# Kernel tuning notes

Hardware: AMD Instinct MI355X
Metric: run time of the kernel (lower is better)

## Reference

```python
import jax, jax.numpy as jnp
import numpy as np
import math

# ---- static configuration (mirrors init_kwargs) ----
NQ = 8            # n_qubits (main register)
NA = 2            # n_ancilla = ceil(log2(n_select))
NSEL = 4          # n_select
DEG = 3           # degree
LAYERS = 2        # n_ansatz_layers
KLOC = 2          # k_local
LATENT = 128
B = 256
NROTS = 4 * NQ * LAYERS          # 64
GROUPS = [(s, s + 1) for s in range(NQ - KLOC + 1)]  # sliding 2-local -> 7 groups
NOBS = len(GROUPS)
KDIM = 2 ** KLOC                  # 4
C64 = jnp.complex64
TWO_PI = 2.0 * math.pi

CNOT = jnp.array([[1, 0, 0, 0], [0, 1, 0, 0], [0, 0, 0, 1], [0, 0, 1, 0]], dtype=C64)

# ---- gate matrices (theta may be traced) ----
def ry_mat(th):
    c = jnp.cos(th / 2).astype(C64); s = jnp.sin(th / 2).astype(C64)
    return jnp.stack([jnp.stack([c, -s]), jnp.stack([s, c])])

def rz_mat(th):
    return jnp.diag(jnp.stack([jnp.exp(-0.5j * th), jnp.exp(0.5j * th)])).astype(C64)

def crx_mat(th):
    c = jnp.cos(th / 2).astype(C64); isn = (-1j * jnp.sin(th / 2)).astype(C64)
    one = jnp.ones((), C64)
    m = jnp.zeros((4, 4), C64)
    m = m.at[0, 0].set(one).at[1, 1].set(one)
    m = m.at[2, 2].set(c).at[3, 3].set(c).at[2, 3].set(isn).at[3, 2].set(isn)
    return m

# ---- state-vector gate application (state: (2,)*rank, wire = axis) ----
def apply_1q(state, U, w):
    return jnp.moveaxis(jnp.tensordot(U, state, axes=((1,), (w,))), 0, w)

def apply_2q(state, U, w0, w1):
    st = jnp.tensordot(U.reshape(2, 2, 2, 2), state, axes=((2, 3), (w0, w1)))
    return jnp.moveaxis(st, (0, 1), (w0, w1))

def _sim14_ops(nq, layers):
    ops, idx = [], 0
    for _ in range(layers):
        for i in range(nq):
            ops.append(("ry", (i,), idx)); idx += 1
        for i in range(nq - 1, -1, -1):
            ops.append(("crx", (i, (i + 1) % nq), idx)); idx += 1
        for i in range(nq):
            ops.append(("ry", (i,), idx)); idx += 1
        for i in [nq - 1] + list(range(nq - 1)):
            ops.append(("crx", (i, (i - 1) % nq), idx)); idx += 1
    return ops

def apply_sim14(state, p, layers, adjoint=False):
    ops = _sim14_ops(NQ, layers)
    seq = list(reversed(ops)) if adjoint else ops
    sgn = -1.0 if adjoint else 1.0
    for kind, ws, idx in seq:
        th = sgn * p[idx]
        if kind == "ry":
            state = apply_1q(state, ry_mat(th), ws[0])
        else:
            state = apply_2q(state, crx_mat(th), ws[0], ws[1])
    return state

def pcphase(state, phi):
    # e^{+i phi} on ancilla=|0..0> subspace (first 2^NQ states in (anc, main) ordering), e^{-i phi} elsewhere
    sr = state.reshape(2 ** NQ, 2 ** NA)
    ph = jnp.where(jnp.arange(2 ** NA) == 0, jnp.exp(1j * phi), jnp.exp(-1j * phi)).astype(C64)
    return (sr * ph[None, :]).reshape(state.shape)

def prepare(state, prep_p, adjoint=False):
    if not adjoint:
        for ly in range(NA):          # n_prep_layers == n_ancilla
            for qi in range(NA):
                state = apply_1q(state, ry_mat(prep_p[ly, qi, 0]), NQ + qi)
                state = apply_1q(state, rz_mat(prep_p[ly, qi, 1]), NQ + qi)
            for i in range(NA - 1):
                state = apply_2q(state, CNOT, NQ + i, NQ + i + 1)
    else:
        for ly in reversed(range(NA)):
            for i in reversed(range(NA - 1)):
                state = apply_2q(state, CNOT, NQ + i, NQ + i + 1)
            for qi in reversed(range(NA)):
                state = apply_1q(state, rz_mat(-prep_p[ly, qi, 1]), NQ + qi)
                state = apply_1q(state, ry_mat(-prep_p[ly, qi, 0]), NQ + qi)
    return state

def select(state, ts, adjoint=False):
    # ancilla wires (NQ, NQ+1) are the trailing axes; flattened index == control value s
    sr = state.reshape((2,) * NQ + (2 ** NA,))
    for s in range(NSEL):
        sub = apply_sim14(sr[..., s], ts[s], LAYERS, adjoint=adjoint)
        sr = sr.at[..., s].set(sub)
    return sr.reshape(state.shape)

def create_hermitian(A, Bp, D, N):
    h = jnp.zeros((N, N), C64)
    count = 0
    for i in range(1, N):
        h = h.at[i - 1, i - 1].set(D[i].astype(C64))
        for j in range(i):
            h = h.at[i, j].set((A[count + j] + 1j * Bp[count + j]).astype(C64))
        count += i
    return h + h.conj().T

def simulate(ts, prep_p, sig, qff, H_all):
    # ts: (NSEL, NROTS) for one batch element
    state = jnp.zeros((2,) * (NQ + NA), C64).at[(0,) * (NQ + NA)].set(1.0)
    state = pcphase(state, sig[0])
    for k in range(DEG):
        state = prepare(state, prep_p)
        state = select(state, ts, adjoint=(k % 2 == 1))
        state = prepare(state, prep_p, adjoint=True)
        state = pcphase(state, sig[k + 1])
    state = apply_sim14(state, qff, 1)
    es = []
    for w, (a, b) in enumerate(GROUPS):
        hpsi = apply_2q(state, H_all[w], a, b)
        es.append(jnp.real(jnp.vdot(state, hpsi)))
    return jnp.stack(es).astype(jnp.float32)  # (NOBS,)

def linear(x, w, b):
    return x @ w.T + b

def sinusoidal_embedding(t, dim):
    half = dim // 2
    freqs = jnp.exp(-math.log(10000.0) * jnp.arange(half, dtype=jnp.float32) / half)
    args = t[:, None] * freqs[None]
    return jnp.concatenate([jnp.cos(args), jnp.sin(args)], axis=-1)

def _forward(z_t, t, te_w1, te_b1, te_w2, te_b2, ip_w1, ip_b1, ip_w2, ip_b2,
             prep_params, signal_angles, qff_params, A_obs, B_obs, D_obs, head_w, head_b):
    t_emb = sinusoidal_embedding(t, LATENT)
    t_emb = linear(jax.nn.silu(linear(t_emb, te_w1, te_b1)), te_w2, te_b2)
    h = jnp.concatenate([z_t, t_emb], axis=-1)
    h = linear(jax.nn.silu(linear(h, ip_w1, ip_b1)), ip_w2, ip_b2)
    ts = jax.nn.sigmoid(h).reshape(z_t.shape[0], NSEL, NROTS) * TWO_PI
    H_all = jax.vmap(lambda a, b, d: create_hermitian(a, b, d, KDIM))(A_obs, B_obs, D_obs)  # (NOBS,4,4)
    expvals = jax.vmap(simulate, in_axes=(0, None, None, None, None))(
        ts, prep_params, signal_angles, qff_params, H_all)  # (B, NOBS)
    return linear(expvals, head_w, head_b)  # (B, LATENT)

def setup_inputs() -> dict:
    key = jax.random.key(0)
    ks = jax.random.split(key, 16)
    def n(k, shape, s=0.05):
        return s * jax.random.normal(k, shape, jnp.float32)
    return {
        "z_t": jax.random.normal(ks[0], (B, LATENT), jnp.float32),
        "t": jax.random.uniform(ks[1], (B,), jnp.float32),
        "te_w1": n(ks[2], (LATENT, LATENT)), "te_b1": jnp.zeros((LATENT,), jnp.float32),
        "te_w2": n(ks[3], (LATENT, LATENT)), "te_b2": jnp.zeros((LATENT,), jnp.float32),
        "ip_w1": n(ks[4], (2 * LATENT, 2 * LATENT)), "ip_b1": jnp.zeros((2 * LATENT,), jnp.float32),
        "ip_w2": n(ks[5], (NSEL * NROTS, 2 * LATENT)), "ip_b2": jnp.zeros((NSEL * NROTS,), jnp.float32),
        "prep_params": 0.1 * jax.random.normal(ks[6], (NA, NA, 2), jnp.float32),
        "signal_angles": 0.1 * jax.random.normal(ks[7], (DEG + 1,), jnp.float32),
        "qff_params": jax.random.uniform(ks[8], (4 * NQ,), jnp.float32),
        "A_obs": 2.0 * jax.random.normal(ks[9], (NOBS, KDIM * (KDIM - 1) // 2), jnp.float32),
        "B_obs": 2.0 * jax.random.normal(ks[10], (NOBS, KDIM * (KDIM - 1) // 2), jnp.float32),
        "D_obs": 2.0 * jax.random.normal(ks[11], (NOBS, KDIM), jnp.float32),
        "head_w": n(ks[12], (LATENT, NOBS)), "head_b": jnp.zeros((LATENT,), jnp.float32),
    }

def reference(z_t, t, te_w1, te_b1, te_w2, te_b2, ip_w1, ip_b1, ip_w2, ip_b2,
              prep_params, signal_angles, qff_params, A_obs, B_obs, D_obs, head_w, head_b):
    return _forward(z_t, t, te_w1, te_b1, te_w2, te_b2, ip_w1, ip_b1, ip_w2, ip_b2,
                    prep_params, signal_angles, qff_params, A_obs, B_obs, D_obs, head_w, head_b)
```

## Files before the change

kernel.cpp:

```cpp
#include <hip/hip_runtime.h>
#include <math.h>

#define NOBS 7
#define PI_F 3.14159265358979f


typedef float v2f __attribute__((ext_vector_type(2)));

__device__ __forceinline__ v2f pk_mul(v2f a, v2f b) {
  v2f d;
  asm("v_pk_mul_f32 %0, %1, %2" : "=v"(d) : "v"(a), "v"(b));
  return d;
}
__device__ __forceinline__ v2f pk_fma(v2f a, v2f b, v2f c) {
  v2f d;
  asm("v_pk_fma_f32 %0, %1, %2, %3" : "=v"(d) : "v"(a), "v"(b), "v"(c));
  return d;
}

template<int LM>
__device__ __forceinline__ float lane_partner(float x) {
  if constexpr (LM == 1) {
    return __int_as_float(__builtin_amdgcn_mov_dpp(__float_as_int(x), 0xB1, 0xF, 0xF, true));
  } else if constexpr (LM == 2) {
    return __int_as_float(__builtin_amdgcn_mov_dpp(__float_as_int(x), 0x4E, 0xF, 0xF, true));
  } else if constexpr (LM == 4) {
    int a = __builtin_amdgcn_mov_dpp(__float_as_int(x), 0x1B, 0xF, 0xF, true);
    return __int_as_float(__builtin_amdgcn_mov_dpp(a, 0x141, 0xF, 0xF, true));
  } else if constexpr (LM == 8) {
    int a = __builtin_amdgcn_mov_dpp(__float_as_int(x), 0x141, 0xF, 0xF, true);
    return __int_as_float(__builtin_amdgcn_mov_dpp(a, 0x140, 0xF, 0xF, true));
  } else if constexpr (LM == 16) {
#if __has_builtin(__builtin_amdgcn_permlane16_swap)
    unsigned xu = __float_as_uint(x);
    auto r = __builtin_amdgcn_permlane16_swap(xu, xu, false, false);
    return (__uint_as_float(r[0]) + __uint_as_float(r[1])) - x;
#else
    return __shfl_xor(x, 16, 64);
#endif
  } else {
#if __has_builtin(__builtin_amdgcn_permlane32_swap)
    unsigned xu = __float_as_uint(x);
    auto r = __builtin_amdgcn_permlane32_swap(xu, xu, false, false);
    return (__uint_as_float(r[0]) + __uint_as_float(r[1])) - x;
#else
    return __shfl_xor(x, 32, 64);
#endif
  }
}

template<int LM>
__device__ __forceinline__ float xor_sum(float x) {
  if constexpr (LM == 16) {
#if __has_builtin(__builtin_amdgcn_permlane16_swap)
    unsigned xu = __float_as_uint(x);
    auto r = __builtin_amdgcn_permlane16_swap(xu, xu, false, false);
    return __uint_as_float(r[0]) + __uint_as_float(r[1]);
#else
    return x + __shfl_xor(x, 16, 64);
#endif
  } else if constexpr (LM == 32) {
#if __has_builtin(__builtin_amdgcn_permlane32_swap)
    unsigned xu = __float_as_uint(x);
    auto r = __builtin_amdgcn_permlane32_swap(xu, xu, false, false);
    return __uint_as_float(r[0]) + __uint_as_float(r[1]);
#else
    return x + __shfl_xor(x, 32, 64);
#endif
  } else {
    return x + lane_partner<LM>(x);
  }
}

__device__ __forceinline__ float rdlane(float v, int idx) {
  return __int_as_float(__builtin_amdgcn_readlane(__float_as_int(v), idx));
}

__device__ __forceinline__ float2 cmul(float2 a, float2 b) {
  return make_float2(a.x*b.x - a.y*b.y, a.x*b.y + a.y*b.x);
}
__device__ __forceinline__ float2 cmulc(float2 a, float2 b) {
  return make_float2(a.x*b.x + a.y*b.y, a.y*b.x - a.x*b.y);
}
__device__ __forceinline__ float2 cadd(float2 a, float2 b) {
  return make_float2(a.x + b.x, a.y + b.y);
}

struct SV { v2f q[4]; };


template<int W>
__device__ __forceinline__ void ry_lane4(v2f* vv, int lane,
                                         float ct, float st, int idx, float sg) {
  float c = rdlane(ct, idx), s = sg * rdlane(st, idx);
  constexpr int LM = 1 << (5 - W);
  const float ls = (lane & LM) ? s : -s;
  v2f c2 = {c, c}, ls2 = {ls, ls};
#pragma unroll
  for (int r = 0; r < 4; ++r) {
    v2f p;
    p.x = lane_partner<LM>(vv[r].x);
    p.y = lane_partner<LM>(vv[r].y);
    vv[r] = pk_fma(ls2, p, pk_mul(c2, vv[r]));
  }
}

__device__ __forceinline__ void ry_reg6(v2f* vv, float ct, float st, int idx, float sg) {
  float c = rdlane(ct, idx), s = sg * rdlane(st, idx);
  v2f c2 = {c, c}, s2 = {s, s}, ns2 = {-s, -s};
#pragma unroll
  for (int k = 0; k < 2; ++k) {
    v2f a0 = vv[k], a1 = vv[k + 2];
    vv[k]     = pk_fma(ns2, a1, pk_mul(c2, a0));
    vv[k + 2] = pk_fma(s2,  a0, pk_mul(c2, a1));
  }
}

__device__ __forceinline__ void ry_reg7(v2f* vv, float ct, float st, int idx, float sg) {
  float c = rdlane(ct, idx), s = sg * rdlane(st, idx);
  v2f c2 = {c, c}, s2 = {s, s}, ns2 = {-s, -s};
#pragma unroll
  for (int k = 0; k < 4; k += 2) {
    v2f a0 = vv[k], a1 = vv[k + 1];
    vv[k]     = pk_fma(ns2, a1, pk_mul(c2, a0));
    vv[k + 1] = pk_fma(s2,  a0, pk_mul(c2, a1));
  }
}

template<int C, int T>
__device__ __forceinline__ void crx_ll4(v2f* vv, int lane,
                                        float ct, float st, int idx, float sg) {
  float c = rdlane(ct, idx), s = sg * rdlane(st, idx);
  constexpr int LC = 1 << (5 - C), LT = 1 << (5 - T);
  const bool act = (lane & LC) != 0;
  const float cp = act ? c : 1.f, sp = act ? s : 0.f;
  v2f cp2 = {cp, cp}, ssp2 = {sp, -sp};
#pragma unroll
  for (int r = 0; r < 4; ++r) {
    v2f p;
    p.x = lane_partner<LT>(vv[r].y);
    p.y = lane_partner<LT>(vv[r].x);
    vv[r] = pk_fma(ssp2, p, pk_mul(cp2, vv[r]));
  }
}

template<int RB, int T>
__device__ __forceinline__ void crx_rc_lane(v2f* vv,
                                            float ct, float st, int idx, float sg) {
  float c = rdlane(ct, idx), s = sg * rdlane(st, idx);
  constexpr int LT = 1 << (5 - T);
  v2f c2 = {c, c}, ss2 = {s, -s};
#pragma unroll
  for (int r = 0; r < 4; ++r) {
    if (r & RB) {
      v2f p;
      p.x = lane_partner<LT>(vv[r].y);
      p.y = lane_partner<LT>(vv[r].x);
      vv[r] = pk_fma(ss2, p, pk_mul(c2, vv[r]));
    }
  }
}

template<int C, int TB>
__device__ __forceinline__ void crx_lc_reg(v2f* vv, int lane,
                                           float ct, float st, int idx, float sg) {
  float c = rdlane(ct, idx), s = sg * rdlane(st, idx);
  constexpr int LC = 1 << (5 - C);
  const bool act = (lane & LC) != 0;
  const float cp = act ? c : 1.f, sp = act ? s : 0.f;
  v2f cp2 = {cp, cp}, ssp2 = {sp, -sp};
#pragma unroll
  for (int x = 0; x < 4; ++x) {
    if (!(x & TB)) {
      const int y = x | TB;
      v2f ox = vv[x], oy = vv[y];
      v2f swx = {ox.y, ox.x}, swy = {oy.y, oy.x};
      vv[x] = pk_fma(ssp2, swy, pk_mul(cp2, ox));
      vv[y] = pk_fma(ssp2, swx, pk_mul(cp2, oy));
    }
  }
}

template<int CB, int TB>
__device__ __forceinline__ void crx_rr(v2f* vv,
                                       float ct, float st, int idx, float sg) {
  float c = rdlane(ct, idx), s = sg * rdlane(st, idx);
  constexpr int x = CB, y = CB | TB;
  v2f c2 = {c, c}, ss2 = {s, -s};
  v2f ox = vv[x], oy = vv[y];
  v2f swx = {ox.y, ox.x}, swy = {oy.y, oy.x};
  vv[x] = pk_fma(ss2, swy, pk_mul(c2, ox));
  vv[y] = pk_fma(ss2, swx, pk_mul(c2, oy));
}


__device__ __forceinline__ SV sim14_fwd(SV v, float ct, float st, int off) {
  const int lane = threadIdx.x & 63;
  v2f* vv = v.q;
  const float sg = 1.f;
  ry_lane4<0>(vv,lane,ct,st,off+0,sg); ry_lane4<1>(vv,lane,ct,st,off+1,sg);
  ry_lane4<2>(vv,lane,ct,st,off+2,sg); ry_lane4<3>(vv,lane,ct,st,off+3,sg);
  ry_lane4<4>(vv,lane,ct,st,off+4,sg); ry_lane4<5>(vv,lane,ct,st,off+5,sg);
  ry_reg6(vv,ct,st,off+6,sg);
  ry_reg7(vv,ct,st,off+7,sg);
  crx_rc_lane<1,0>(vv,ct,st,off+8,sg);
  crx_rr<2,1>(vv,ct,st,off+9,sg);
  crx_lc_reg<5,2>(vv,lane,ct,st,off+10,sg);
  crx_ll4<4,5>(vv,lane,ct,st,off+11,sg); crx_ll4<3,4>(vv,lane,ct,st,off+12,sg);
  crx_ll4<2,3>(vv,lane,ct,st,off+13,sg); crx_ll4<1,2>(vv,lane,ct,st,off+14,sg);
  crx_ll4<0,1>(vv,lane,ct,st,off+15,sg);
  ry_lane4<0>(vv,lane,ct,st,off+16,sg); ry_lane4<1>(vv,lane,ct,st,off+17,sg);
  ry_lane4<2>(vv,lane,ct,st,off+18,sg); ry_lane4<3>(vv,lane,ct,st,off+19,sg);
  ry_lane4<4>(vv,lane,ct,st,off+20,sg); ry_lane4<5>(vv,lane,ct,st,off+21,sg);
  ry_reg6(vv,ct,st,off+22,sg);
  ry_reg7(vv,ct,st,off+23,sg);
  crx_rr<1,2>(vv,ct,st,off+24,sg);
  crx_lc_reg<0,1>(vv,lane,ct,st,off+25,sg);
  crx_ll4<1,0>(vv,lane,ct,st,off+26,sg); crx_ll4<2,1>(vv,lane,ct,st,off+27,sg);
  crx_ll4<3,2>(vv,lane,ct,st,off+28,sg); crx_ll4<4,3>(vv,lane,ct,st,off+29,sg);
  crx_ll4<5,4>(vv,lane,ct,st,off+30,sg);
  crx_rc_lane<2,5>(vv,ct,st,off+31,sg);
  return v;
}

__device__ __forceinline__ SV sim14_adj(SV v, float ct, float st, int off) {
  const int lane = threadIdx.x & 63;
  v2f* vv = v.q;
  const float sg = -1.f;
  crx_rc_lane<2,5>(vv,ct,st,off+31,sg);
  crx_ll4<5,4>(vv,lane,ct,st,off+30,sg); crx_ll4<4,3>(vv,lane,ct,st,off+29,sg);
  crx_ll4<3,2>(vv,lane,ct,st,off+28,sg); crx_ll4<2,1>(vv,lane,ct,st,off+27,sg);
  crx_ll4<1,0>(vv,lane,ct,st,off+26,sg);
  crx_lc_reg<0,1>(vv,lane,ct,st,off+25,sg);
  crx_rr<1,2>(vv,ct,st,off+24,sg);
  ry_reg7(vv,ct,st,off+23,sg);
  ry_reg6(vv,ct,st,off+22,sg);
  ry_lane4<5>(vv,lane,ct,st,off+21,sg); ry_lane4<4>(vv,lane,ct,st,off+20,sg);
  ry_lane4<3>(vv,lane,ct,st,off+19,sg); ry_lane4<2>(vv,lane,ct,st,off+18,sg);
  ry_lane4<1>(vv,lane,ct,st,off+17,sg); ry_lane4<0>(vv,lane,ct,st,off+16,sg);
  crx_ll4<0,1>(vv,lane,ct,st,off+15,sg); crx_ll4<1,2>(vv,lane,ct,st,off+14,sg);
  crx_ll4<2,3>(vv,lane,ct,st,off+13,sg); crx_ll4<3,4>(vv,lane,ct,st,off+12,sg);
  crx_ll4<4,5>(vv,lane,ct,st,off+11,sg);
  crx_lc_reg<5,2>(vv,lane,ct,st,off+10,sg);
  crx_rr<2,1>(vv,ct,st,off+9,sg);
  crx_rc_lane<1,0>(vv,ct,st,off+8,sg);
  ry_reg7(vv,ct,st,off+7,sg);
  ry_reg6(vv,ct,st,off+6,sg);
  ry_lane4<5>(vv,lane,ct,st,off+5,sg); ry_lane4<4>(vv,lane,ct,st,off+4,sg);
  ry_lane4<3>(vv,lane,ct,st,off+3,sg); ry_lane4<2>(vv,lane,ct,st,off+2,sg);
  ry_lane4<1>(vv,lane,ct,st,off+1,sg); ry_lane4<0>(vv,lane,ct,st,off+0,sg);
  return v;
}


template<int IN, int NP, int MODE>
__device__ __forceinline__ void mlp_layer(const float* __restrict__ W,
    const float* __restrict__ bias, const float* xl, float* yl,
    int rbase, int lane)
{
  const int sub = lane & 7;
  const int g   = lane >> 3;
#pragma unroll
  for (int p = 0; p < NP; ++p) {
    const int row = rbase + p * 8 + g;
    const float4* w4 = (const float4*)(W + row * IN) + sub;
    const float4* x4 = (const float4*)xl + sub;
    v2f acc2 = {0.f, 0.f};
#pragma unroll
    for (int it = 0; it < IN / 32; ++it) {
      float4 w = w4[it * 8], e = x4[it * 8];
      v2f wa = {w.x, w.y}, wb = {w.z, w.w};
      v2f ea = {e.x, e.y}, eb = {e.z, e.w};
      acc2 = pk_fma(wa, ea, acc2);
      acc2 = pk_fma(wb, eb, acc2);
    }
    float acc = acc2.x + acc2.y;
    acc = xor_sum<1>(acc);
    acc = xor_sum<2>(acc);
    acc = xor_sum<4>(acc);
    if (sub == 0) {
      float a = acc + bias[row];
      if constexpr (MODE == 0) {
        yl[row] = a / (1.f + __expf(-a));
      } else if constexpr (MODE == 1) {
        yl[row] = a;
      } else {
        float th = PI_F / (1.f + __expf(-a));
        float sn, cn;
        __sincosf(th, &sn, &cn);
        ((float2*)yl)[row] = make_float2(cn, sn);
      }
    }
  }
}


__global__ __launch_bounds__(256, 1) void qsvt_kernel(
    const float* __restrict__ z_t, const float* __restrict__ t,
    const float* __restrict__ te_w1, const float* __restrict__ te_b1,
    const float* __restrict__ te_w2, const float* __restrict__ te_b2,
    const float* __restrict__ ip_w1, const float* __restrict__ ip_b1,
    const float* __restrict__ ip_w2, const float* __restrict__ ip_b2,
    const float* __restrict__ prep_p, const float* __restrict__ sig,
    const float* __restrict__ qff,
    const float* __restrict__ A_obs, const float* __restrict__ B_obs,
    const float* __restrict__ D_obs,
    const float* __restrict__ head_w, const float* __restrict__ head_b,
    float* __restrict__ out)
{
  __shared__ __align__(16) float emb[128];
  __shared__ __align__(16) float y1[128];
  __shared__ __align__(16) float hbuf[256];
  __shared__ __align__(16) float h1[256];
  __shared__ __align__(16) float2 seltab[256];
  __shared__ __align__(16) float2 qtab2[32];
  __shared__ __align__(16) float2 sX1[16], sX2[16], sF[16], sa0[4];
  __shared__ __align__(16) float dumpR[4][256];
  __shared__ __align__(16) float dumpI[4][256];
  __shared__ float redbuf[NOBS][4];
  __shared__ float hdc[NOBS][3], hxc[NOBS][6], hyc[NOBS][6];
  __shared__ __align__(16) float shw[128 * NOBS];
  __shared__ __align__(16) float shb[128];
  extern __shared__ float4 dxw[];

  const int tid  = threadIdx.x;
  const int lane = tid & 63;
  const int wv   = tid >> 6;
  const int s    = wv;
  const int b    = blockIdx.x;

  if (tid < 32) {
    float sn, cn;
    __sincosf(0.5f * qff[tid], &sn, &cn);
    qtab2[tid] = make_float2(cn, sn);
  }
  if (wv == 0) {
    float2 Ga[2][2][2], Gb[2][2][2];
    for (int ly = 0; ly < 2; ++ly)
      for (int qi = 0; qi < 2; ++qi) {
        float y = prep_p[ly*4 + qi*2 + 0], z = prep_p[ly*4 + qi*2 + 1];
        float cy, sy, cz, sz;
        __sincosf(0.5f*y, &sy, &cy);
        __sincosf(0.5f*z, &sz, &cz);
        float2 g00 = make_float2( cy*cz, -cy*sz);
        float2 g01 = make_float2(-sy*cz,  sy*sz);
        float2 g10 = make_float2( sy*cz,  sy*sz);
        float2 g11 = make_float2( cy*cz,  cy*sz);
        if (qi == 0) { Ga[ly][0][0]=g00; Ga[ly][0][1]=g01; Ga[ly][1][0]=g10; Ga[ly][1][1]=g11; }
        else         { Gb[ly][0][0]=g00; Gb[ly][0][1]=g01; Gb[ly][1][0]=g10; Gb[ly][1][1]=g11; }
      }
    float2 M[2][4][4];
    for (int ly = 0; ly < 2; ++ly) {
      float2 T[4][4];
      for (int i = 0; i < 4; ++i)
        for (int j = 0; j < 4; ++j)
          T[i][j] = cmul(Ga[ly][i>>1][j>>1], Gb[ly][i&1][j&1]);
      for (int j = 0; j < 4; ++j) {
        M[ly][0][j] = T[0][j]; M[ly][1][j] = T[1][j];
        M[ly][2][j] = T[3][j]; M[ly][3][j] = T[2][j];
      }
    }
    float2 U[4][4];
    for (int i = 0; i < 4; ++i)
      for (int j = 0; j < 4; ++j) {
        float2 acc = make_float2(0.f, 0.f);
        for (int kk = 0; kk < 4; ++kk) acc = cadd(acc, cmul(M[1][i][kk], M[0][kk][j]));
        U[i][j] = acc;
      }
    float c0n, s0n, c1, s1v, c2, s2v, c3, s3v;
    __sincosf(sig[0], &s0n, &c0n);
    __sincosf(sig[1], &s1v, &c1);
    __sincosf(sig[2], &s2v, &c2);
    __sincosf(sig[3], &s3v, &c3);
    if (lane < 16) {
      int i = lane >> 2, j = lane & 3;
      float2 a1 = make_float2(0.f, 0.f), a2 = make_float2(0.f, 0.f);
      for (int k = 0; k < 4; ++k) {
        float2 tt = cmulc(U[i][k], U[j][k]);
        float sk = (k == 0) ? 1.f : -1.f;
        a1 = cadd(a1, cmul(tt, make_float2(c1, sk*s1v)));
        a2 = cadd(a2, cmul(tt, make_float2(c2, sk*s2v)));
      }
      sX1[lane] = a1;
      sX2[lane] = a2;
      float2 d3 = make_float2(c3, (i == 0) ? s3v : -s3v);
      sF[lane] = cmul(d3, make_float2(U[j][i].x, -U[j][i].y));
    }
    if (lane < 4) sa0[lane] = cmul(U[lane][0], make_float2(c0n, s0n));
  }

  if (tid < 128) {
    float fr = __expf(-9.210340371976184f * (float)(tid & 63) / 64.f);
    float arg = t[b] * fr;
    float sn, cn;
    __sincosf(arg, &sn, &cn);
    emb[tid] = (tid < 64) ? cn : sn;
  }
  __syncthreads();

  mlp_layer<128, 4, 0>(te_w1, te_b1, emb, y1, wv * 32, lane);
  if (tid < 128) hbuf[tid] = z_t[b * 128 + tid];
  __syncthreads();

  mlp_layer<128, 4, 1>(te_w2, te_b2, y1, hbuf + 128, wv * 32, lane);
  __syncthreads();

  mlp_layer<256, 8, 0>(ip_w1, ip_b1, hbuf, h1, wv * 64, lane);
  __syncthreads();

  mlp_layer<256, 8, 2>(ip_w2, ip_b2, h1, (float*)seltab, wv * 64, lane);

  if (tid < NOBS * 6)      { hxc[tid/6][tid%6] = A_obs[tid]; hyc[tid/6][tid%6] = B_obs[tid]; }
  else if (tid >= 64 && tid < 64 + NOBS*3) { int q = tid - 64; hdc[q/3][q%3] = 2.f * D_obs[(q/3)*4 + (q%3) + 1]; }
#pragma unroll
  for (int i = tid; i < 128*NOBS; i += 256) shw[i] = head_w[i];
  if (tid < 128) shb[tid] = head_b[tid];
  __syncthreads();

  float2 mycs = seltab[(s << 6) | lane];
  float selc = mycs.x, sels = mycs.y;
  float2 myq = qtab2[lane & 31];
  float qc = myq.x, qs = myq.y;

  SV v;
#pragma unroll
  for (int r = 0; r < 4; ++r) { v.q[r].x = 0.f; v.q[r].y = 0.f; }
  if (lane == 0) {
    float2 a0 = sa0[s];
    v.q[0].x = a0.x; v.q[0].y = a0.y;
  }

  auto ancmix = [&](const float2* R, int site) {
    float4* bufR = dxw + (site & 1) * 512;
    float4* bufI = bufR + 256;
    bufR[wv * 64 + lane] = make_float4(v.q[0].x, v.q[1].x, v.q[2].x, v.q[3].x);
    bufI[wv * 64 + lane] = make_float4(v.q[0].y, v.q[1].y, v.q[2].y, v.q[3].y);
    __syncthreads();
    float outr[4] = {0.f, 0.f, 0.f, 0.f}, outi[4] = {0.f, 0.f, 0.f, 0.f};
#pragma unroll
    for (int sp = 0; sp < 4; ++sp) {
      float4 Pr = bufR[sp * 64 + lane];
      float4 Pi = bufI[sp * 64 + lane];
      float2 Rr = R[sp];
      outr[0] += Rr.x*Pr.x - Rr.y*Pi.x;  outi[0] += Rr.x*Pi.x + Rr.y*Pr.x;
      outr[1] += Rr.x*Pr.y - Rr.y*Pi.y;  outi[1] += Rr.x*Pi.y + Rr.y*Pr.y;
      outr[2] += Rr.x*Pr.z - Rr.y*Pi.z;  outi[2] += Rr.x*Pi.z + Rr.y*Pr.z;
      outr[3] += Rr.x*Pr.w - Rr.y*Pi.w;  outi[3] += Rr.x*Pi.w + Rr.y*Pr.w;
    }
#pragma unroll
    for (int r = 0; r < 4; ++r) { v.q[r].x = outr[r]; v.q[r].y = outi[r]; }
  };

  v = sim14_fwd(v, selc, sels, 0);
  v = sim14_fwd(v, selc, sels, 32);
  ancmix(&sX1[s << 2], 0);
  v = sim14_adj(v, selc, sels, 32);
  v = sim14_adj(v, selc, sels, 0);
  ancmix(&sX2[s << 2], 1);
  v = sim14_fwd(v, selc, sels, 0);
  v = sim14_fwd(v, selc, sels, 32);
  ancmix(&sF[s << 2], 2);
  v = sim14_fwd(v, qc, qs, 0);

  *(float4*)&dumpR[s][lane << 2] = make_float4(v.q[0].x, v.q[1].x, v.q[2].x, v.q[3].x);
  *(float4*)&dumpI[s][lane << 2] = make_float4(v.q[0].y, v.q[1].y, v.q[2].y, v.q[3].y);

#pragma unroll
  for (int w = 0; w < NOBS; ++w) {
    const int pb = 6 - w;
    int g = lane;
    int ib = ((g >> pb) << (pb + 2)) | (g & ((1 << pb) - 1));
    float xr[4], xi[4];
#pragma unroll
    for (int i = 0; i < 4; ++i) { xr[i] = dumpR[s][ib + (i << pb)]; xi[i] = dumpI[s][ib + (i << pb)]; }
    float a = hdc[w][0] * (xr[0]*xr[0] + xi[0]*xi[0])
            + hdc[w][1] * (xr[1]*xr[1] + xi[1]*xi[1])
            + hdc[w][2] * (xr[2]*xr[2] + xi[2]*xi[2]);
    const int oi[6] = {1, 2, 2, 3, 3, 3};
    const int oj[6] = {0, 0, 1, 0, 1, 2};
#pragma unroll
    for (int k2 = 0; k2 < 6; ++k2) {
      int i = oi[k2], j = oj[k2];
      float rr = xr[i]*xr[j] + xi[i]*xi[j];
      float ii = xr[i]*xi[j] - xi[i]*xr[j];
      a += 2.f * (hxc[w][k2]*rr - hyc[w][k2]*ii);
    }
    a = xor_sum<32>(a);
    a = xor_sum<16>(a);
    a = xor_sum<8>(a);
    a = xor_sum<4>(a);
    a = xor_sum<2>(a);
    a = xor_sum<1>(a);
    if (lane == 0) redbuf[w][s] = a;
  }
  __syncthreads();

  if (tid < 128) {
    float acc = shb[tid];
#pragma unroll
    for (int w = 0; w < NOBS; ++w) {
      float ev = redbuf[w][0] + redbuf[w][1] + redbuf[w][2] + redbuf[w][3];
      acc += ev * shw[tid*NOBS + w];
    }
    out[b * 128 + tid] = acc;
  }
}

extern "C" void kernel_launch(void* const* d_in, const int* in_sizes, int n_in,
                              void* d_out, int out_size, void* d_ws, size_t ws_size,
                              hipStream_t stream) {
  (void)n_in; (void)out_size; (void)d_ws; (void)ws_size;
  const float* z_t    = (const float*)d_in[0];
  const float* t      = (const float*)d_in[1];
  const float* te_w1  = (const float*)d_in[2];
  const float* te_b1  = (const float*)d_in[3];
  const float* te_w2  = (const float*)d_in[4];
  const float* te_b2  = (const float*)d_in[5];
  const float* ip_w1  = (const float*)d_in[6];
  const float* ip_b1  = (const float*)d_in[7];
  const float* ip_w2  = (const float*)d_in[8];
  const float* ip_b2  = (const float*)d_in[9];
  const float* prep_p = (const float*)d_in[10];
  const float* sig    = (const float*)d_in[11];
  const float* qff    = (const float*)d_in[12];
  const float* A_obs  = (const float*)d_in[13];
  const float* B_obs  = (const float*)d_in[14];
  const float* D_obs  = (const float*)d_in[15];
  const float* head_w = (const float*)d_in[16];
  const float* head_b = (const float*)d_in[17];
  float* out = (float*)d_out;

  int B = in_sizes[1];
  size_t dyn = 2 * 512 * sizeof(float4);
  qsvt_kernel<<<B, 256, dyn, stream>>>(
      z_t, t, te_w1, te_b1, te_w2, te_b2, ip_w1, ip_b1, ip_w2, ip_b2,
      prep_p, sig, qff, A_obs, B_obs, D_obs, head_w, head_b, out);
}
```

Measured before the change: 124.1 us.

## Process two batch elements per 512-thread block

Each block now handles two batch elements with 512 threads, so the grid is halved and the per-block setup (gate tables, observable coefficients, head weights) is shared across two samples. Shared buffers are duplicated per element and a clamped batch index guards an odd batch size. With B=256 the grid shrinks to 128 blocks, which may underfill a 256-CU device, and the block-wide barriers now couple the two elements.

New measurement: 158.0 us. +27.3%, slower.

```diff
diff --git a/kernel.cpp b/kernel.cpp
--- a/kernel.cpp
+++ b/kernel.cpp
@@ -295,7 +295,7 @@
 }
 
 
-__global__ __launch_bounds__(256, 1) void qsvt_kernel(
+__global__ __launch_bounds__(512, 1) void qsvt_kernel(
     const float* __restrict__ z_t, const float* __restrict__ t,
     const float* __restrict__ te_w1, const float* __restrict__ te_b1,
     const float* __restrict__ te_w2, const float* __restrict__ te_b2,
@@ -306,18 +306,18 @@
     const float* __restrict__ A_obs, const float* __restrict__ B_obs,
     const float* __restrict__ D_obs,
     const float* __restrict__ head_w, const float* __restrict__ head_b,
-    float* __restrict__ out)
+    float* __restrict__ out, int B)
 {
-  __shared__ __align__(16) float emb[128];
-  __shared__ __align__(16) float y1[128];
-  __shared__ __align__(16) float hbuf[256];
-  __shared__ __align__(16) float h1[256];
-  __shared__ __align__(16) float2 seltab[256];
+  __shared__ __align__(16) float emb[2][128];
+  __shared__ __align__(16) float y1[2][128];
+  __shared__ __align__(16) float hbuf[2][256];
+  __shared__ __align__(16) float h1[2][256];
+  __shared__ __align__(16) float2 seltab[2][256];
   __shared__ __align__(16) float2 qtab2[32];
   __shared__ __align__(16) float2 sX1[16], sX2[16], sF[16], sa0[4];
-  __shared__ __align__(16) float dumpR[4][256];
-  __shared__ __align__(16) float dumpI[4][256];
-  __shared__ float redbuf[NOBS][4];
+  __shared__ __align__(16) float dumpR[2][4][256];
+  __shared__ __align__(16) float dumpI[2][4][256];
+  __shared__ float redbuf[2][NOBS][4];
   __shared__ float hdc[NOBS][3], hxc[NOBS][6], hyc[NOBS][6];
   __shared__ __align__(16) float shw[128 * NOBS];
   __shared__ __align__(16) float shb[128];
@@ -326,8 +326,10 @@
   const int tid  = threadIdx.x;
   const int lane = tid & 63;
   const int wv   = tid >> 6;
-  const int s    = wv;
-  const int b    = blockIdx.x;
+  const int e    = wv >> 2;
+  const int s    = wv & 3;
+  const int b    = blockIdx.x * 2 + e;
+  const int bc   = (b < B) ? b : (B - 1);
 
   if (tid < 32) {
     float sn, cn;
@@ -389,35 +391,43 @@
     if (lane < 4) sa0[lane] = cmul(U[lane][0], make_float2(c0n, s0n));
   }
 
-  if (tid < 128) {
-    float fr = __expf(-9.210340371976184f * (float)(tid & 63) / 64.f);
-    float arg = t[b] * fr;
+  if (tid < 256) {
+    const int el = tid >> 7, idx = tid & 127;
+    const int bb = blockIdx.x * 2 + el;
+    const int bcl = (bb < B) ? bb : (B - 1);
+    float fr = __expf(-9.210340371976184f * (float)(idx & 63) / 64.f);
+    float arg = t[bcl] * fr;
     float sn, cn;
     __sincosf(arg, &sn, &cn);
-    emb[tid] = (tid < 64) ? cn : sn;
+    emb[el][idx] = (idx < 64) ? cn : sn;
   }
   __syncthreads();
 
-  mlp_layer<128, 4, 0>(te_w1, te_b1, emb, y1, wv * 32, lane);
-  if (tid < 128) hbuf[tid] = z_t[b * 128 + tid];
+  mlp_layer<128, 4, 0>(te_w1, te_b1, emb[e], y1[e], s * 32, lane);
+  if (tid < 256) {
+    const int el = tid >> 7, idx = tid & 127;
+    const int bb = blockIdx.x * 2 + el;
+    const int bcl = (bb < B) ? bb : (B - 1);
+    hbuf[el][idx] = z_t[bcl * 128 + idx];
+  }
   __syncthreads();
 
-  mlp_layer<128, 4, 1>(te_w2, te_b2, y1, hbuf + 128, wv * 32, lane);
+  mlp_layer<128, 4, 1>(te_w2, te_b2, y1[e], hbuf[e] + 128, s * 32, lane);
   __syncthreads();
 
-  mlp_layer<256, 8, 0>(ip_w1, ip_b1, hbuf, h1, wv * 64, lane);
+  mlp_layer<256, 8, 0>(ip_w1, ip_b1, hbuf[e], h1[e], s * 64, lane);
   __syncthreads();
 
-  mlp_layer<256, 8, 2>(ip_w2, ip_b2, h1, (float*)seltab, wv * 64, lane);
+  mlp_layer<256, 8, 2>(ip_w2, ip_b2, h1[e], (float*)seltab[e], s * 64, lane);
 
   if (tid < NOBS * 6)      { hxc[tid/6][tid%6] = A_obs[tid]; hyc[tid/6][tid%6] = B_obs[tid]; }
   else if (tid >= 64 && tid < 64 + NOBS*3) { int q = tid - 64; hdc[q/3][q%3] = 2.f * D_obs[(q/3)*4 + (q%3) + 1]; }
 #pragma unroll
-  for (int i = tid; i < 128*NOBS; i += 256) shw[i] = head_w[i];
-  if (tid < 128) shb[tid] = head_b[tid];
+  for (int i = tid; i < 128*NOBS; i += 512) shw[i] = head_w[i];
+  if (tid >= 256 && tid < 384) shb[tid - 256] = head_b[tid - 256];
   __syncthreads();
 
-  float2 mycs = seltab[(s << 6) | lane];
+  float2 mycs = seltab[e][(s << 6) | lane];
   float selc = mycs.x, sels = mycs.y;
   float2 myq = qtab2[lane & 31];
   float qc = myq.x, qs = myq.y;
@@ -431,10 +441,10 @@
   }
 
   auto ancmix = [&](const float2* R, int site) {
-    float4* bufR = dxw + (site & 1) * 512;
+    float4* bufR = dxw + e * 1024 + (site & 1) * 512;
     float4* bufI = bufR + 256;
-    bufR[wv * 64 + lane] = make_float4(v.q[0].x, v.q[1].x, v.q[2].x, v.q[3].x);
-    bufI[wv * 64 + lane] = make_float4(v.q[0].y, v.q[1].y, v.q[2].y, v.q[3].y);
+    bufR[s * 64 + lane] = make_float4(v.q[0].x, v.q[1].x, v.q[2].x, v.q[3].x);
+    bufI[s * 64 + lane] = make_float4(v.q[0].y, v.q[1].y, v.q[2].y, v.q[3].y);
     __syncthreads();
     float outr[4] = {0.f, 0.f, 0.f, 0.f}, outi[4] = {0.f, 0.f, 0.f, 0.f};
 #pragma unroll
@@ -462,8 +472,8 @@
   ancmix(&sF[s << 2], 2);
   v = sim14_fwd(v, qc, qs, 0);
 
-  *(float4*)&dumpR[s][lane << 2] = make_float4(v.q[0].x, v.q[1].x, v.q[2].x, v.q[3].x);
-  *(float4*)&dumpI[s][lane << 2] = make_float4(v.q[0].y, v.q[1].y, v.q[2].y, v.q[3].y);
+  *(float4*)&dumpR[e][s][lane << 2] = make_float4(v.q[0].x, v.q[1].x, v.q[2].x, v.q[3].x);
+  *(float4*)&dumpI[e][s][lane << 2] = make_float4(v.q[0].y, v.q[1].y, v.q[2].y, v.q[3].y);
 
 #pragma unroll
   for (int w = 0; w < NOBS; ++w) {
@@ -472,7 +482,7 @@
     int ib = ((g >> pb) << (pb + 2)) | (g & ((1 << pb) - 1));
     float xr[4], xi[4];
 #pragma unroll
-    for (int i = 0; i < 4; ++i) { xr[i] = dumpR[s][ib + (i << pb)]; xi[i] = dumpI[s][ib + (i << pb)]; }
+    for (int i = 0; i < 4; ++i) { xr[i] = dumpR[e][s][ib + (i << pb)]; xi[i] = dumpI[e][s][ib + (i << pb)]; }
     float a = hdc[w][0] * (xr[0]*xr[0] + xi[0]*xi[0])
             + hdc[w][1] * (xr[1]*xr[1] + xi[1]*xi[1])
             + hdc[w][2] * (xr[2]*xr[2] + xi[2]*xi[2]);
@@ -491,18 +501,22 @@
     a = xor_sum<4>(a);
     a = xor_sum<2>(a);
     a = xor_sum<1>(a);
-    if (lane == 0) redbuf[w][s] = a;
+    if (lane == 0) redbuf[e][w][s] = a;
   }
   __syncthreads();
 
-  if (tid < 128) {
-    float acc = shb[tid];
-#pragma unroll
-    for (int w = 0; w < NOBS; ++w) {
-      float ev = redbuf[w][0] + redbuf[w][1] + redbuf[w][2] + redbuf[w][3];
-      acc += ev * shw[tid*NOBS + w];
-    }
-    out[b * 128 + tid] = acc;
+  if (tid < 256) {
+    const int el = tid >> 7, idx = tid & 127;
+    const int bb = blockIdx.x * 2 + el;
+    if (bb < B) {
+      float acc = shb[idx];
+#pragma unroll
+      for (int w = 0; w < NOBS; ++w) {
+        float ev = redbuf[el][w][0] + redbuf[el][w][1] + redbuf[el][w][2] + redbuf[el][w][3];
+        acc += ev * shw[idx*NOBS + w];
+      }
+      out[bb * 128 + idx] = acc;
+    }
   }
 }
 
@@ -531,8 +545,9 @@
   float* out = (float*)d_out;
 
   int B = in_sizes[1];
-  size_t dyn = 2 * 512 * sizeof(float4);
-  qsvt_kernel<<<B, 256, dyn, stream>>>(
+  int nb = (B + 1) / 2;
+  size_t dyn = 2 * 1024 * sizeof(float4);
+  qsvt_kernel<<<nb, 512, dyn, stream>>>(
       z_t, t, te_w1, te_b1, te_w2, te_b2, ip_w1, ip_b1, ip_w2, ip_b2,
-      prep_p, sig, qff, A_obs, B_obs, D_obs, head_w, head_b, out);
-}
+      prep_p, sig, qff, A_obs, B_obs, D_obs, head_w, head_b, out, B);
+}
```
